# Performance work log

Measured on AMD Instinct MI355X. Metric: run time of the kernel, lower is better.

The kernel has to match this reference:

```python
import jax, jax.numpy as jnp
import numpy as np

DN = ('NCHW', 'OIHW', 'NCHW')

def _conv(x, w, groups=1, padding=0):
    return jax.lax.conv_general_dilated(
        x, w, window_strides=(1, 1), padding=[(padding, padding)] * 2,
        dimension_numbers=DN, feature_group_count=groups)

def _bn(x, scale, shift):
    # precomputed inference BN: x * scale + shift, per channel (NCHW)
    return x * scale[None, :, None, None] + shift[None, :, None, None]

def _channel_shuffle(x, g):
    n, c, h, w = x.shape
    return x.reshape(n, g, c // g, h, w).transpose(0, 2, 1, 3, 4).reshape(n, c, h, w)

def setup_inputs() -> dict:
    key = jax.random.key(0)
    ks = jax.random.split(key, 13)
    N, Cin, H, W = 32, 240, 56, 56
    Cout, G = 480, 3
    mid = Cout // 4  # 120
    inp = {
        'x': jax.random.normal(ks[0], (N, Cin, H, W), jnp.float32),
        'w1': jax.random.normal(ks[1], (mid, Cin // G, 1, 1), jnp.float32) * 0.05,
        'scale1': jax.random.uniform(ks[2], (mid,), jnp.float32, 0.5, 1.5),
        'shift1': jax.random.normal(ks[3], (mid,), jnp.float32) * 0.1,
        'w2': jax.random.normal(ks[4], (mid, 1, 3, 3), jnp.float32) * 0.05,
        'scale2': jax.random.uniform(ks[5], (mid,), jnp.float32, 0.5, 1.5),
        'shift2': jax.random.normal(ks[6], (mid,), jnp.float32) * 0.1,
        'w3': jax.random.normal(ks[7], (Cout, mid // G, 1, 1), jnp.float32) * 0.05,
        'scale3': jax.random.uniform(ks[8], (Cout,), jnp.float32, 0.5, 1.5),
        'shift3': jax.random.normal(ks[9], (Cout,), jnp.float32) * 0.1,
        'wsc': jax.random.normal(ks[10], (Cout, Cin, 1, 1), jnp.float32) * 0.05,
        'scale_sc': jax.random.uniform(ks[11], (Cout,), jnp.float32, 0.5, 1.5),
        'shift_sc': jax.random.normal(ks[12], (Cout,), jnp.float32) * 0.1,
        'groups': G,
    }
    return inp

def reference(x, w1, scale1, shift1, w2, scale2, shift2, w3, scale3, shift3,
              wsc, scale_sc, shift_sc, groups):
    g = int(groups)
    mid = w1.shape[0]
    # conv1 (grouped 1x1) -> fused BN + ReLU
    y = _conv(x, w1, groups=g)
    y = jax.nn.relu(_bn(y, scale1, shift1))
    # conv2 (depthwise 3x3) -> fused BN + channel shuffle
    y = _conv(y, w2, groups=mid, padding=1)
    y = _channel_shuffle(_bn(y, scale2, shift2), g)
    # conv3 (grouped 1x1)
    y = _conv(y, w3, groups=g)
    # shortcut: 1x1 conv (in_channels != out_channels)
    z = _conv(x, wsc)
    # fused final: relu(BN3(y)) + BN_sc(z)
    return jax.nn.relu(_bn(y, scale3, shift3)) + _bn(z, scale_sc, shift_sc)
```

## Files before the change

kernel.cpp:

```cpp
#include <hip/hip_runtime.h>

typedef short bf16x8 __attribute__((ext_vector_type(8)));
typedef float f32x4 __attribute__((ext_vector_type(4)));
typedef unsigned int u32x4 __attribute__((ext_vector_type(4)));

namespace {
constexpr int kHW = 3136;
constexpr int kNPx = 32 * kHW;
constexpr int kPtiles = kNPx / 16;
constexpr size_t kXbiShorts = (size_t)kPtiles * 4096;
constexpr size_t kY2iShorts = (size_t)kPtiles * 2048;
}

__device__ __align__(16) unsigned short g_w1i[3 * 4 * 48 * 32];
__device__ __align__(16) unsigned short g_wsci[8 * 480 * 32];
__device__ __align__(16) unsigned short g_w3i[2 * 480 * 32];
__device__ __align__(16) float g_w2f[9 * 120];

static __device__ __forceinline__ unsigned short f2b(float f) {
  unsigned u = __float_as_uint(f);
  u = (u + 0x7fffu + ((u >> 16) & 1u)) >> 16;
  return (unsigned short)u;
}
static __device__ __forceinline__ float b2f(unsigned short u) {
  return __uint_as_float((unsigned)u << 16);
}
static __device__ __forceinline__ f32x4 mfma16(bf16x8 a, bf16x8 b, f32x4 c) {
  return __builtin_amdgcn_mfma_f32_16x16x32_bf16(a, b, c, 0, 0, 0);
}
static __device__ __forceinline__ bf16x8 ldg8(const unsigned short* p) {
  return *reinterpret_cast<const bf16x8*>(p);
}

__global__ __launch_bounds__(256) void prep_weights(
    const float* __restrict__ w1, const float* __restrict__ wsc,
    const float* __restrict__ w3, const float* __restrict__ w2,
    const float* __restrict__ scale2) {
  const int idx = blockIdx.x * 256 + threadIdx.x;
  if (idx < 18432) {
    const int g = idx / 6144, r = idx % 6144, kb = r / 1536;
    const int j = (r % 1536) / 32, k = r % 32;
    const int gk = g * 64 + kb * 32 + k;
    const int c = gk - g * 80;
    unsigned short v = 0;
    if (j < 40 && c >= 0 && c < 80) v = f2b(w1[(g * 40 + j) * 80 + c]);
    g_w1i[idx] = v;
  } else if (idx < 18432 + 122880) {
    const int i = idx - 18432;
    const int kb = i / 15360, co = (i % 15360) / 32, k = i % 32;
    const int c = kb * 32 + k;
    g_wsci[i] = (c < 240) ? f2b(wsc[co * 240 + c]) : (unsigned short)0;
  } else if (idx < 18432 + 122880 + 30720) {
    const int i = idx - 141312;
    const int kb = i / 15360, co = (i % 15360) / 32, k = i % 32;
    const int cb = co / 160;
    const int s = cb * 32 + kb * 32 + k - cb * 40;
    g_w3i[i] = (s >= 0 && s < 40) ? f2b(w3[co * 40 + s]) : (unsigned short)0;
  } else if (idx < 18432 + 122880 + 30720 + 1080) {
    const int i = idx - 172032;
    const int tap = i / 120, c = i % 120;
    g_w2f[i] = w2[c * 9 + tap] * scale2[c];
  }
}

__global__ __launch_bounds__(256) void t_conv1(
    const float* __restrict__ x, const float* __restrict__ scale1,
    const float* __restrict__ shift1, unsigned short* __restrict__ xbi,
    unsigned short* __restrict__ y1) {
  const int P0 = blockIdx.x * 64;
  const int lane = threadIdx.x & 63;
  const int wv = threadIdx.x >> 6;
  const int l15 = lane & 15, part = lane >> 4;
  const size_t PT = (size_t)(P0 / 16) + wv;
  const int px = P0 + wv * 16 + l15;
  const int n = px / kHW, hw = px % kHW;

  __shared__ unsigned short lds_y1[64 * 120];

  bf16x8 pk[8];
  const float* xp = x + (size_t)n * 240 * kHW + hw;
  unsigned short* gdst = xbi + PT * 4096 + l15 * 32 + part * 8;
#pragma unroll
  for (int kb = 0; kb < 8; ++kb) {
    bf16x8 t;
#pragma unroll
    for (int j = 0; j < 8; ++j) {
      const int c = kb * 32 + part * 8 + j;
      t[j] = (c < 240)
                 ? (short)f2b(__builtin_nontemporal_load(xp + (size_t)c * kHW))
                 : (short)0;
    }
    pk[kb] = t;
    __builtin_nontemporal_store(__builtin_bit_cast(u32x4, t),
                                reinterpret_cast<u32x4*>(gdst + kb * 512));
  }

  const int quad = part;
#pragma unroll
  for (int g = 0; g < 3; ++g) {
    f32x4 acc[3];
#pragma unroll
    for (int nt = 0; nt < 3; ++nt) acc[nt] = (f32x4){0.f, 0.f, 0.f, 0.f};
#pragma unroll
    for (int kb = 0; kb < 4; ++kb) {
      const bf16x8 A = pk[2 * g + kb];
#pragma unroll
      for (int nt = 0; nt < 3; ++nt) {
        const bf16x8 B = ldg8(g_w1i + (((g * 4 + kb) * 48) + nt * 16 + l15) * 32 +
                              quad * 8);
        acc[nt] = mfma16(A, B, acc[nt]);
      }
    }
#pragma unroll
    for (int nt = 0; nt < 3; ++nt) {
      const int j = nt * 16 + l15;
      if (j < 40) {
        const int c = g * 40 + j;
        const float sc = scale1[c], sh = shift1[c];
#pragma unroll
        for (int r = 0; r < 4; ++r) {
          float v = fmaf(acc[nt][r], sc, sh);
          v = v > 0.f ? v : 0.f;
          lds_y1[(wv * 16 + quad * 4 + r) * 120 + c] = f2b(v);
        }
      }
    }
  }
  __syncthreads();

  unsigned short* yo = y1 + (size_t)P0 * 120;
  for (int q = threadIdx.x; q < 960; q += 256) {
    *reinterpret_cast<uint4*>(yo + q * 8) =
        *reinterpret_cast<const uint4*>(lds_y1 + q * 8);
  }
}

__global__ __launch_bounds__(256) void dw_shuffle(
    const unsigned short* __restrict__ y1, const float* __restrict__ shift2,
    unsigned short* __restrict__ y2i) {
  const int pt = blockIdx.x;
  const int t = threadIdx.x;
  __shared__ float lds_y2[16 * 121];

  if (t < 240) {
    const int px_l = t / 15, m = t % 15;
    const int c0 = m * 8;
    const int px = pt * 16 + px_l;
    const int n = px / kHW, hw = px % kHW;
    const int h = hw / 56, w = hw % 56;

    float acc[8];
    {
      const float4 s0 = *reinterpret_cast<const float4*>(shift2 + c0);
      const float4 s1 = *reinterpret_cast<const float4*>(shift2 + c0 + 4);
      acc[0] = s0.x; acc[1] = s0.y; acc[2] = s0.z; acc[3] = s0.w;
      acc[4] = s1.x; acc[5] = s1.y; acc[6] = s1.z; acc[7] = s1.w;
    }
    const unsigned short* yb = y1 + (size_t)n * kHW * 120 + c0;
#pragma unroll
    for (int dy = 0; dy < 3; ++dy) {
      const int hh = h + dy - 1;
      if (hh >= 0 && hh < 56) {
#pragma unroll
        for (int dx = 0; dx < 3; ++dx) {
          const int ww = w + dx - 1;
          if (ww >= 0 && ww < 56) {
            const bf16x8 v = ldg8(yb + (size_t)(hh * 56 + ww) * 120);
            const float* wp = g_w2f + (dy * 3 + dx) * 120 + c0;
            float wv_[8];
            *reinterpret_cast<float4*>(wv_) =
                *reinterpret_cast<const float4*>(wp);
            *reinterpret_cast<float4*>(wv_ + 4) =
                *reinterpret_cast<const float4*>(wp + 4);
#pragma unroll
            for (int j = 0; j < 8; ++j)
              acc[j] = fmaf(b2f((unsigned short)v[j]), wv_[j], acc[j]);
          }
        }
      }
    }
#pragma unroll
    for (int j = 0; j < 8; ++j) lds_y2[px_l * 121 + c0 + j] = acc[j];
  }
  __syncthreads();

  const int q = t * 8;
  const int kb = q >> 9, r = q & 511, pxl = r >> 5, k0 = r & 31;
  unsigned short v[8];
#pragma unroll
  for (int j = 0; j < 8; ++j) {
    const int cn = kb * 32 + k0 + j;
    const int c = (cn % 3) * 40 + cn / 3;
    v[j] = (cn < 120) ? f2b(lds_y2[pxl * 121 + c]) : (unsigned short)0;
  }
  *reinterpret_cast<uint4*>(y2i + (size_t)pt * 2048 + q) =
      *reinterpret_cast<const uint4*>(v);
}

__global__ __launch_bounds__(256, 4) void conv3_sc_gemm(
    const unsigned short* __restrict__ xbi,
    const unsigned short* __restrict__ y2i, const float* __restrict__ scale3,
    const float* __restrict__ shift3, const float* __restrict__ ssc,
    const float* __restrict__ bsc, float* __restrict__ out) {
  const int bid = blockIdx.x;
  const int l = (bid & 7) * 588 + (bid >> 3);
  const int pxb = l / 3;
  const int cb = l % 3;
  const int P0 = pxb * 64;
  const int lane = threadIdx.x & 63;
  const int wv = threadIdx.x >> 6;
  const int mh = wv & 1, nh = wv >> 1;
  const int l15 = lane & 15, quad = lane >> 4;
  const int cbase = cb * 160 + nh * 80;

  f32x4 acc[2][5];
#pragma unroll
  for (int mt = 0; mt < 2; ++mt)
#pragma unroll
    for (int nt = 0; nt < 5; ++nt) acc[mt][nt] = (f32x4){0.f, 0.f, 0.f, 0.f};

  const size_t PT = (size_t)(P0 / 16) + mh * 2;

#pragma unroll
  for (int kb = 0; kb < 2; ++kb) {
    const int kbi = cb + kb;
    bf16x8 A[2];
#pragma unroll
    for (int mt = 0; mt < 2; ++mt)
      A[mt] = ldg8(y2i + (PT + mt) * 2048 + kbi * 512 + l15 * 32 + quad * 8);
#pragma unroll
    for (int nt = 0; nt < 5; ++nt) {
      const bf16x8 B =
          ldg8(g_w3i + ((kb * 480) + cbase + nt * 16 + l15) * 32 + quad * 8);
#pragma unroll
      for (int mt = 0; mt < 2; ++mt) acc[mt][nt] = mfma16(A[mt], B, acc[mt][nt]);
    }
  }

#pragma unroll
  for (int nt = 0; nt < 5; ++nt) {
    const int co = cbase + nt * 16 + l15;
    const float s3 = scale3[co], h3 = shift3[co];
    const float is = 1.0f / ssc[co], h_ = bsc[co];
#pragma unroll
    for (int mt = 0; mt < 2; ++mt)
#pragma unroll
      for (int r = 0; r < 4; ++r) {
        float v3 = fmaf(acc[mt][nt][r], s3, h3);
        v3 = v3 > 0.f ? v3 : 0.f;
        acc[mt][nt][r] = (v3 + h_) * is;
      }
  }

#pragma unroll 2
  for (int kb = 0; kb < 8; ++kb) {
    bf16x8 A[2];
#pragma unroll
    for (int mt = 0; mt < 2; ++mt)
      A[mt] = ldg8(xbi + (PT + mt) * 4096 + kb * 512 + l15 * 32 + quad * 8);
#pragma unroll
    for (int nt = 0; nt < 5; ++nt) {
      const bf16x8 B =
          ldg8(g_wsci + ((kb * 480) + cbase + nt * 16 + l15) * 32 + quad * 8);
#pragma unroll
      for (int mt = 0; mt < 2; ++mt) acc[mt][nt] = mfma16(A[mt], B, acc[mt][nt]);
    }
  }

#pragma unroll
  for (int mt = 0; mt < 2; ++mt) {
    const int P = P0 + mh * 32 + mt * 16 + quad * 4;
    const int n = P / kHW, hw = P % kHW;
    float* ob = out + (size_t)n * 480 * kHW + hw;
#pragma unroll
    for (int nt = 0; nt < 5; ++nt) {
      const int co = cbase + nt * 16 + l15;
      const float s_ = ssc[co];
      f32x4 r;
#pragma unroll
      for (int r4 = 0; r4 < 4; ++r4) r[r4] = s_ * acc[mt][nt][r4];
      __builtin_nontemporal_store(
          r, reinterpret_cast<f32x4*>(ob + (size_t)co * kHW));
    }
  }
}

extern "C" void kernel_launch(void* const* d_in, const int* in_sizes, int n_in,
                              void* d_out, int out_size, void* d_ws,
                              size_t ws_size, hipStream_t stream) {
  const float* x = (const float*)d_in[0];
  const float* w1 = (const float*)d_in[1];
  const float* scale1 = (const float*)d_in[2];
  const float* shift1 = (const float*)d_in[3];
  const float* w2 = (const float*)d_in[4];
  const float* scale2 = (const float*)d_in[5];
  const float* shift2 = (const float*)d_in[6];
  const float* w3 = (const float*)d_in[7];
  const float* scale3 = (const float*)d_in[8];
  const float* shift3 = (const float*)d_in[9];
  const float* wsc = (const float*)d_in[10];
  const float* ssc = (const float*)d_in[11];
  const float* bsc = (const float*)d_in[12];
  float* out = (float*)d_out;

  unsigned short* xbi = (unsigned short*)d_ws;
  unsigned short* y2i = xbi + kXbiShorts;
  unsigned short* y1 = y2i + kY2iShorts;

  prep_weights<<<677, 256, 0, stream>>>(w1, wsc, w3, w2, scale2);
  t_conv1<<<kNPx / 64, 256, 0, stream>>>(x, scale1, shift1, xbi, y1);
  dw_shuffle<<<kPtiles, 256, 0, stream>>>(y1, shift2, y2i);
  conv3_sc_gemm<<<1568 * 3, 256, 0, stream>>>(xbi, y2i, scale3, shift3, ssc,
                                              bsc, out);
}
```

Baseline: 466.2 us.

## Retile conv3+shortcut GEMM to 512 pixels by 32 channels per block

Changes the block tile of the fused conv3/shortcut GEMM from 64 pixels × 160 channels to 512 pixels × 32 channels. Each wave now does 8 M-tiles × 2 N-tiles, reusing each weight fragment across 8 pixel tiles. The XCD-aware block remapping is adjusted for the new grid of 2940 blocks. The aim is to cut redundant weight loads and reshape the per-block work. The cost is that each activation tile is re-read by 15 channel-group blocks instead of 3, which leans on L2 reuse.

After: 444.0 us. -4.8%, faster.

```diff
diff --git a/kernel.cpp b/kernel.cpp
--- a/kernel.cpp
+++ b/kernel.cpp
@@ -203,47 +203,48 @@
     const float* __restrict__ shift3, const float* __restrict__ ssc,
     const float* __restrict__ bsc, float* __restrict__ out) {
   const int bid = blockIdx.x;
-  const int l = (bid & 7) * 588 + (bid >> 3);
-  const int pxb = l / 3;
-  const int cb = l % 3;
-  const int P0 = pxb * 64;
+  const int xcd = bid & 7, i = bid >> 3;
+  const int l = (xcd < 4 ? xcd * 368 : 4 * 368 + (xcd - 4) * 367) + i;
+  const int pxg = l / 15;
+  const int cog = l % 15;
+  const int cb = cog / 5;
+  const int cbase = cog * 32;
   const int lane = threadIdx.x & 63;
   const int wv = threadIdx.x >> 6;
-  const int mh = wv & 1, nh = wv >> 1;
   const int l15 = lane & 15, quad = lane >> 4;
-  const int cbase = cb * 160 + nh * 80;
-
-  f32x4 acc[2][5];
-#pragma unroll
-  for (int mt = 0; mt < 2; ++mt)
-#pragma unroll
-    for (int nt = 0; nt < 5; ++nt) acc[mt][nt] = (f32x4){0.f, 0.f, 0.f, 0.f};
-
-  const size_t PT = (size_t)(P0 / 16) + mh * 2;
+
+  f32x4 acc[8][2];
+#pragma unroll
+  for (int mt = 0; mt < 8; ++mt)
+#pragma unroll
+    for (int nt = 0; nt < 2; ++nt) acc[mt][nt] = (f32x4){0.f, 0.f, 0.f, 0.f};
+
+  const size_t PT = (size_t)pxg * 32 + wv * 8;
 
 #pragma unroll
   for (int kb = 0; kb < 2; ++kb) {
     const int kbi = cb + kb;
-    bf16x8 A[2];
-#pragma unroll
-    for (int mt = 0; mt < 2; ++mt)
-      A[mt] = ldg8(y2i + (PT + mt) * 2048 + kbi * 512 + l15 * 32 + quad * 8);
-#pragma unroll
-    for (int nt = 0; nt < 5; ++nt) {
-      const bf16x8 B =
+    bf16x8 B[2];
+#pragma unroll
+    for (int nt = 0; nt < 2; ++nt)
+      B[nt] =
           ldg8(g_w3i + ((kb * 480) + cbase + nt * 16 + l15) * 32 + quad * 8);
 #pragma unroll
-      for (int mt = 0; mt < 2; ++mt) acc[mt][nt] = mfma16(A[mt], B, acc[mt][nt]);
-    }
-  }
-
-#pragma unroll
-  for (int nt = 0; nt < 5; ++nt) {
+    for (int mt = 0; mt < 8; ++mt) {
+      const bf16x8 A =
+          ldg8(y2i + (PT + mt) * 2048 + kbi * 512 + l15 * 32 + quad * 8);
+#pragma unroll
+      for (int nt = 0; nt < 2; ++nt) acc[mt][nt] = mfma16(A, B[nt], acc[mt][nt]);
+    }
+  }
+
+#pragma unroll
+  for (int nt = 0; nt < 2; ++nt) {
     const int co = cbase + nt * 16 + l15;
     const float s3 = scale3[co], h3 = shift3[co];
     const float is = 1.0f / ssc[co], h_ = bsc[co];
 #pragma unroll
-    for (int mt = 0; mt < 2; ++mt)
+    for (int mt = 0; mt < 8; ++mt)
 #pragma unroll
       for (int r = 0; r < 4; ++r) {
         float v3 = fmaf(acc[mt][nt][r], s3, h3);
@@ -254,26 +255,27 @@
 
 #pragma unroll 2
   for (int kb = 0; kb < 8; ++kb) {
-    bf16x8 A[2];
-#pragma unroll
-    for (int mt = 0; mt < 2; ++mt)
-      A[mt] = ldg8(xbi + (PT + mt) * 4096 + kb * 512 + l15 * 32 + quad * 8);
-#pragma unroll
-    for (int nt = 0; nt < 5; ++nt) {
-      const bf16x8 B =
+    bf16x8 B[2];
+#pragma unroll
+    for (int nt = 0; nt < 2; ++nt)
+      B[nt] =
           ldg8(g_wsci + ((kb * 480) + cbase + nt * 16 + l15) * 32 + quad * 8);
 #pragma unroll
-      for (int mt = 0; mt < 2; ++mt) acc[mt][nt] = mfma16(A[mt], B, acc[mt][nt]);
-    }
-  }
-
-#pragma unroll
-  for (int mt = 0; mt < 2; ++mt) {
-    const int P = P0 + mh * 32 + mt * 16 + quad * 4;
+    for (int mt = 0; mt < 8; ++mt) {
+      const bf16x8 A =
+          ldg8(xbi + (PT + mt) * 4096 + kb * 512 + l15 * 32 + quad * 8);
+#pragma unroll
+      for (int nt = 0; nt < 2; ++nt) acc[mt][nt] = mfma16(A, B[nt], acc[mt][nt]);
+    }
+  }
+
+#pragma unroll
+  for (int mt = 0; mt < 8; ++mt) {
+    const int P = pxg * 512 + wv * 128 + mt * 16 + quad * 4;
     const int n = P / kHW, hw = P % kHW;
     float* ob = out + (size_t)n * 480 * kHW + hw;
 #pragma unroll
-    for (int nt = 0; nt < 5; ++nt) {
+    for (int nt = 0; nt < 2; ++nt) {
       const int co = cbase + nt * 16 + l15;
       const float s_ = ssc[co];
       f32x4 r;
@@ -310,6 +312,6 @@
   prep_weights<<<677, 256, 0, stream>>>(w1, wsc, w3, w2, scale2);
   t_conv1<<<kNPx / 64, 256, 0, stream>>>(x, scale1, shift1, xbi, y1);
   dw_shuffle<<<kPtiles, 256, 0, stream>>>(y1, shift2, y2i);
-  conv3_sc_gemm<<<1568 * 3, 256, 0, stream>>>(xbi, y2i, scale3, shift3, ssc,
-                                              bsc, out);
-}
+  conv3_sc_gemm<<<2940, 256, 0, stream>>>(xbi, y2i, scale3, shift3, ssc,
+                                          bsc, out);
+}
```
